# Performance work log

Hardware: AMD Instinct MI355X
Metric: run time of the kernel (lower is better)

Reference implementation:

```python
import jax, jax.numpy as jnp
import numpy as np
from jax import lax

S_IN = 16; V_IN = 16; S_OUT = 16; V_OUT = 16
SIZE = 7; STRIDE = 2; PAD = 3; EPS = 1e-5
# n_basis per (rep_out, rep_in) pair = n_radial(3) * number of allowed CG paths
NB = {('s','s'): 3, ('s','v'): 3, ('s','t'): 9, ('v','s'): 3, ('v','v'): 9, ('v','t'): 21}
DIMS = {'s': 1, 'v': 3, 't': 9}  # repr1, repr3, repr3x3 dimensions


def _basis(key, nb, d_out, d_in):
    # Stand-in for the constant steerable basis (spherical harmonics x Clebsch-Gordan
    # x radial windows). These are data-independent constants in se3cnn; the compute
    # pattern (weighted basis sum -> dense 3D conv) is identical.
    return jax.random.normal(key, (nb, d_out, d_in, SIZE, SIZE, SIZE), jnp.float32) / np.sqrt(SIZE ** 3)


def setup_inputs() -> dict:
    key = jax.random.key(0)
    ks = jax.random.split(key, 16)
    inp = {"sv": jax.random.normal(ks[0], (4, S_IN + 3 * V_IN, 32, 32, 32), jnp.float32)}
    mul_in = {'s': S_IN, 'v': V_IN, 't': V_IN}
    i = 1
    for o in ['s', 'v']:
        mo = S_OUT if o == 's' else V_OUT
        for a in ['s', 'v', 't']:
            nb = NB[(o, a)]
            inp[f"basis_{o}{a}"] = _basis(ks[i], nb, DIMS[o], DIMS[a])
            inp[f"w_{o}{a}"] = jax.random.normal(ks[i + 1], (mo, mul_in[a], nb), jnp.float32) / np.sqrt(nb * mul_in[a] * DIMS[a])
            i += 2
    inp["bn_g_s"] = jnp.ones((S_OUT,), jnp.float32)
    inp["bn_g_v"] = jnp.ones((V_OUT,), jnp.float32)
    inp["bias_s"] = jnp.zeros((S_OUT,), jnp.float32)
    return inp


def _block(w, basis):
    # w: [mul_out, mul_in, nb], basis: [nb, d_out, d_in, 7,7,7] -> [mul_out*d_out, mul_in*d_in, 7,7,7]
    mo, mi, nb = w.shape
    do, di = basis.shape[1], basis.shape[2]
    k = jnp.einsum('uvb,bijxyz->uivjxyz', w, basis)
    return k.reshape(mo * do, mi * di, SIZE, SIZE, SIZE)


def _forward(sv, w_ss, w_sv, w_st, w_vs, w_vv, w_vt,
             basis_ss, basis_sv, basis_st, basis_vs, basis_vv, basis_vt,
             bn_g_s, bn_g_v, bias_s):
    B = sv.shape[0]; sp = sv.shape[2:]
    # TensorProduct: vector fields -> vector (x) vector = repr3x3 (9 channels each)
    v = sv[:, S_IN:].reshape(B, V_IN, 3, *sp)
    t = jnp.einsum('buixyz,bujxyz->buijxyz', v, v).reshape(B, V_IN * 9, *sp)
    svt = jnp.concatenate([sv, t], axis=1)  # [B, S_IN + 3*V_IN + 9*V_IN, X,Y,Z]
    # SE3Convolution: assemble kernel from steerable basis, then dense 3D conv
    row_s = jnp.concatenate([_block(w_ss, basis_ss), _block(w_sv, basis_sv), _block(w_st, basis_st)], axis=1)
    row_v = jnp.concatenate([_block(w_vs, basis_vs), _block(w_vv, basis_vv), _block(w_vt, basis_vt)], axis=1)
    kernel = jnp.concatenate([row_s, row_v], axis=0)  # [S_OUT + 3*V_OUT, 208, 7,7,7]
    y = lax.conv_general_dilated(svt, kernel, (STRIDE,) * 3, [(PAD, PAD)] * 3,
                                 dimension_numbers=('NCDHW', 'OIDHW', 'NCDHW'))
    osp = y.shape[2:]
    # SE3BatchNorm: per-field second-moment normalization (training-mode batch stats)
    ys = y[:, :S_OUT]
    yv = y[:, S_OUT:].reshape(B, V_OUT, 3, *osp)
    var_s = jnp.mean(ys * ys, axis=(0, 2, 3, 4))
    ys = ys * (bn_g_s / jnp.sqrt(var_s + EPS))[None, :, None, None, None]
    var_v = jnp.mean(yv * yv, axis=(0, 2, 3, 4, 5))
    yv = yv * (bn_g_v / jnp.sqrt(var_v + EPS))[None, :, None, None, None, None]
    # BiasRelu: bias + relu on scalar fields only; vector fields pass through
    ys = jax.nn.relu(ys + bias_s[None, :, None, None, None])
    return jnp.concatenate([ys, yv.reshape(B, 3 * V_OUT, *osp)], axis=1)


def reference(sv, w_ss, w_sv, w_st, w_vs, w_vv, w_vt,
              basis_ss, basis_sv, basis_st, basis_vs, basis_vv, basis_vt,
              bn_g_s, bn_g_v, bias_s):
    return _forward(sv, w_ss, w_sv, w_st, w_vs, w_vv, w_vt,
                    basis_ss, basis_sv, basis_st, basis_vs, basis_vv, basis_vt,
                    bn_g_s, bn_g_v, bias_s)
```

## Files before the change

### kernel.cpp

```cpp
#include <hip/hip_runtime.h>
#include <hip/hip_bf16.h>


using f4  = __attribute__((ext_vector_type(4)))  float;
using f16v= __attribute__((ext_vector_type(16))) float;
using s8  = __attribute__((ext_vector_type(8)))  short;

#define C_TOT 160
#define PZ_   37
#define NTAP  343
#define NROW  (4 * PZ_ * PZ_)
#define KSN   8
#define SLICE_E 1048576

#define AROW    1232
#define AE_ROWS 19
#define AO_ROWS 18
#define AO_OFF  23552
#define B_OFF   46080
#define BSZ     14336
#define LDS_SZ  (B_OFF + 2 * BSZ)

__device__ __forceinline__ void gl_lds16(const void* g, void* l) {
    __builtin_amdgcn_global_load_lds(
        (const __attribute__((address_space(1))) unsigned int*)g,
        (__attribute__((address_space(3))) unsigned int*)l, 16, 0, 0);
}

__device__ __forceinline__ void pair_ij(int p, int& i, int& j) {
    if (p < 3)      { i = p; j = p; }
    else if (p == 3){ i = 0; j = 1; }
    else if (p == 4){ i = 0; j = 2; }
    else            { i = 1; j = 2; }
}

struct bf2 { __hip_bfloat16 x, y; };
struct bh4 { __hip_bfloat16 x, y, z, w; };

__global__ void build_w_kernel(
    const float* __restrict__ b_ss, const float* __restrict__ w_ss,
    const float* __restrict__ b_sv, const float* __restrict__ w_sv,
    const float* __restrict__ b_st, const float* __restrict__ w_st,
    const float* __restrict__ b_vs, const float* __restrict__ w_vs,
    const float* __restrict__ b_vv, const float* __restrict__ w_vv,
    const float* __restrict__ b_vt, const float* __restrict__ w_vt,
    __hip_bfloat16* __restrict__ wl)
{
    __shared__ float S[13056];
    const int tid = threadIdx.x;
    const int tap = blockIdx.x;
    float* L = S;
    float* W = S + 768;
    for (int r = tid; r < 750; r += 192) {
        float v;
        if (r < 3)        v = b_ss[r * NTAP + tap];
        else if (r < 12)  v = b_sv[(r - 3) * NTAP + tap];
        else if (r < 93)  v = b_st[(r - 12) * NTAP + tap];
        else if (r < 102) v = b_vs[(r - 93) * NTAP + tap];
        else if (r < 183) v = b_vv[(r - 102) * NTAP + tap];
        else              v = b_vt[(r - 183) * NTAP + tap];
        L[r] = v;
    }
    for (int r = tid; r < 12288; r += 192) {
        float v;
        if (r < 768)       v = w_ss[r];
        else if (r < 1536) v = w_sv[r - 768];
        else if (r < 3840) v = w_st[r - 1536];
        else if (r < 4608) v = w_vs[r - 3840];
        else if (r < 6912) v = w_vv[r - 4608];
        else               v = w_vt[r - 6912];
        W[r] = v;
    }
    __syncthreads();

    if (tid < 160) {
        const int c = tid;
        const int chunk = c >> 4, cw = c & 15;
        __hip_bfloat16* dst = wl + ((size_t)chunk * NTAP + tap) * 1024 + cw;

        if (c < 16) {
            const float l0 = L[0], l1 = L[1], l2 = L[2];
#pragma unroll
            for (int n = 0; n < 16; ++n) {
                const float* wr = &W[(n * 16 + c) * 3];
                dst[n * 16] = __float2bfloat16(wr[0]*l0 + wr[1]*l1 + wr[2]*l2);
            }
            float bv[3][3];
#pragma unroll
            for (int dn = 0; dn < 3; ++dn)
#pragma unroll
                for (int t = 0; t < 3; ++t) bv[dn][t] = L[93 + t*3 + dn];
#pragma unroll
            for (int u = 0; u < 16; ++u) {
                const float* wr = &W[3840 + (u * 16 + c) * 3];
                const float w0 = wr[0], w1 = wr[1], w2 = wr[2];
#pragma unroll
                for (int dn = 0; dn < 3; ++dn)
                    dst[(16 + u*3 + dn) * 16] = __float2bfloat16(
                        w0*bv[dn][0] + w1*bv[dn][1] + w2*bv[dn][2]);
            }
        } else if (c < 64) {
            const int mm = (c - 16) / 3, di = (c - 16) % 3;
            float bs0[3];
#pragma unroll
            for (int t = 0; t < 3; ++t) bs0[t] = L[3 + t*3 + di];
#pragma unroll
            for (int n = 0; n < 16; ++n) {
                const float* wr = &W[768 + (n * 16 + mm) * 3];
                dst[n * 16] = __float2bfloat16(
                    wr[0]*bs0[0] + wr[1]*bs0[1] + wr[2]*bs0[2]);
            }
            float bv[3][9];
#pragma unroll
            for (int dn = 0; dn < 3; ++dn)
#pragma unroll
                for (int t = 0; t < 9; ++t)
                    bv[dn][t] = L[102 + (t*3 + dn)*3 + di];
#pragma unroll
            for (int u = 0; u < 16; ++u) {
                const float* wr = &W[4608 + (u * 16 + mm) * 9];
                float a0 = 0.f, a1 = 0.f, a2 = 0.f;
#pragma unroll
                for (int t = 0; t < 9; ++t) {
                    const float wv = wr[t];
                    a0 += wv * bv[0][t]; a1 += wv * bv[1][t]; a2 += wv * bv[2][t];
                }
                dst[(16 + u*3 + 0) * 16] = __float2bfloat16(a0);
                dst[(16 + u*3 + 1) * 16] = __float2bfloat16(a1);
                dst[(16 + u*3 + 2) * 16] = __float2bfloat16(a2);
            }
        } else {
            const int q = c - 64, mm = q / 6, p = q % 6;
            int i, jj; pair_ij(p, i, jj);
            const int d1 = i*3 + jj, d2 = jj*3 + i;
            const bool dbl = (i != jj);
            float bs0[9];
#pragma unroll
            for (int t = 0; t < 9; ++t) {
                float b = L[12 + t*9 + d1];
                if (dbl) b += L[12 + t*9 + d2];
                bs0[t] = b;
            }
#pragma unroll
            for (int n = 0; n < 16; ++n) {
                const float* wr = &W[1536 + (n * 16 + mm) * 9];
                float acc = 0.f;
#pragma unroll
                for (int t = 0; t < 9; ++t) acc += wr[t] * bs0[t];
                dst[n * 16] = __float2bfloat16(acc);
            }
            float bv0[21], bv1[21], bv2[21];
#pragma unroll
            for (int t = 0; t < 21; ++t) {
                float x0 = L[183 + (t*3 + 0)*9 + d1];
                float x1 = L[183 + (t*3 + 1)*9 + d1];
                float x2 = L[183 + (t*3 + 2)*9 + d1];
                if (dbl) {
                    x0 += L[183 + (t*3 + 0)*9 + d2];
                    x1 += L[183 + (t*3 + 1)*9 + d2];
                    x2 += L[183 + (t*3 + 2)*9 + d2];
                }
                bv0[t] = x0; bv1[t] = x1; bv2[t] = x2;
            }
#pragma unroll
            for (int u = 0; u < 16; ++u) {
                const float* wr = &W[6912 + (u * 16 + mm) * 21];
                float a0 = 0.f, a1 = 0.f, a2 = 0.f;
#pragma unroll
                for (int t = 0; t < 21; ++t) {
                    const float wv = wr[t];
                    a0 += wv * bv0[t]; a1 += wv * bv1[t]; a2 += wv * bv2[t];
                }
                dst[(16 + u*3 + 0) * 16] = __float2bfloat16(a0);
                dst[(16 + u*3 + 1) * 16] = __float2bfloat16(a1);
                dst[(16 + u*3 + 2) * 16] = __float2bfloat16(a2);
            }
        }
    }
}

__global__ void build_xt_kernel(
    const float* __restrict__ sv, __hip_bfloat16* __restrict__ xt)
{
    __shared__ float row[2112];
    const int tid = threadIdx.x;
    const int bid = blockIdx.x;
    const int y = bid % 37, z = (bid / 37) % 37, b = bid / 1369;
    const bool interior = (z >= 3 && z < 35 && y >= 3 && y < 35);
    if (interior) {
        const float* src = sv + (size_t)b * 2097152 + (z-3) * 1024 + (y-3) * 32;
        for (int f = tid; f < 2048; f += 256) {
            int ch = f >> 5, x = f & 31;
            row[x * 66 + ch] = src[(size_t)ch * 32768 + x];
        }
    }
    __syncthreads();
    for (int e2 = tid; e2 < 3040; e2 += 256) {
        const int chunk = e2 / 304;
        const int r     = e2 - chunk * 304;
        const int s     = r >> 3;
        const int cw    = (r & 7) * 2;
        const int c     = chunk * 16 + cw;
        float v0 = 0.f, v1 = 0.f;
        if (interior && s >= 3 && s < 35) {
            const int x = s - 3;
            if (c < 64) {
                v0 = row[x * 66 + c];
                v1 = row[x * 66 + c + 1];
            } else {
                int q = c - 64, u = q / 6, p = q % 6, i, j;
                pair_ij(p, i, j);
                v0 = row[x * 66 + 16 + u * 3 + i] * row[x * 66 + 16 + u * 3 + j];
                pair_ij(p + 1, i, j);
                v1 = row[x * 66 + 16 + u * 3 + i] * row[x * 66 + 16 + u * 3 + j];
            }
        }
        bf2 w{__float2bfloat16(v0), __float2bfloat16(v1)};
        *(bf2*)(xt + ((size_t)chunk * NROW + bid) * 608 + r * 2) = w;
    }
}

__global__ __launch_bounds__(256, 2) void conv_mfma_kernel(
    const __hip_bfloat16* __restrict__ xt,
    const __hip_bfloat16* __restrict__ wl,
    __hip_bfloat16* __restrict__ y4b)
{
    __shared__ __align__(16) char lds[LDS_SZ];

    const int phys = blockIdx.x;
    const int bid  = (phys & 7) * (64 * KSN / 8) + (phys >> 3);

    const int low3 = bid & 7;
    const int rest = bid >> 3;
    const int ks   = rest % KSN;
    const int mb   = (rest / KSN) * 8 + low3;
    const int b    = mb >> 4;
    const int oz   = mb & 15;

    const int tid  = threadIdx.x;
    const int w    = tid >> 6;
    const int lane = tid & 63;
    const int m    = lane & 31;
    const int h    = lane >> 5;

    int invAE[6]; int nAE = 0;
#pragma unroll
    for (int k = 0; k < 6; ++k) {
        const int i = w + 4 * k;
        if (i < 23) {
            const int o = i * 1024 + lane * 16;
            int r = o / AROW;
            int rem = o - r * AROW;
            if (r > AE_ROWS - 1) { r = AE_ROWS - 1; rem = 0; }
            if (rem >= 1216) rem = 0;
            const int s  = rem >> 5;
            const int cg = ((rem >> 4) & 1) ^ ((s >> 1) & 1);
            invAE[k] = (2 * r) * 608 + s * 16 + cg * 8;
            nAE = k + 1;
        }
    }
    int invAO[6]; int nAO = 0;
#pragma unroll
    for (int k = 0; k < 6; ++k) {
        const int i = w + 4 * k;
        if (i < 22) {
            const int o = i * 1024 + lane * 16;
            int r = o / AROW;
            int rem = o - r * AROW;
            if (r > AO_ROWS - 1) { r = AO_ROWS - 1; rem = 0; }
            if (rem >= 1216) rem = 0;
            const int s  = rem >> 5;
            const int cg = ((rem >> 4) & 1) ^ ((s >> 1) & 1);
            invAO[k] = (2 * r + 1) * 608 + s * 16 + cg * 8;
            nAO = k + 1;
        }
    }
    int invB[4]; int nB = 0;
#pragma unroll
    for (int k = 0; k < 4; ++k) {
        const int i = w + 4 * k;
        if (i < 14) {
            const int kx = i >> 1, nt = i & 1;
            invB[k] = kx * 1024 + (nt * 32 + m) * 16 + h * 8;
            nB = k + 1;
        }
    }

    f16v acc[2][2];
    for (int t = 0; t < 2; ++t)
        for (int n = 0; n < 2; ++n)
            for (int k = 0; k < 16; ++k) acc[t][n][k] = 0.f;

    const int rA0   = ((m >> 4) << 2) + ((m >> 2) & 3);
    const int sbase = (w << 3) + ((m & 3) << 1);

    auto stageAE = [&](int g) {
        const int chunk = g / 7, kz = g - chunk * 7;
        const size_t u = ((size_t)chunk * NROW
                        + (size_t)(b * PZ_ + 2 * oz + kz) * PZ_) * 608;
#pragma unroll
        for (int k = 0; k < 6; ++k)
            if (k < nAE) gl_lds16(xt + u + invAE[k], lds + (w + 4 * k) * 1024);
    };
    auto stageAO = [&](int g) {
        const int chunk = g / 7, kz = g - chunk * 7;
        const size_t u = ((size_t)chunk * NROW
                        + (size_t)(b * PZ_ + 2 * oz + kz) * PZ_) * 608;
#pragma unroll
        for (int k = 0; k < 6; ++k)
            if (k < nAO) gl_lds16(xt + u + invAO[k], lds + AO_OFF + (w + 4 * k) * 1024);
    };
    auto stageB = [&](int g, int kyv, int bsel) {
        const int chunk = g / 7, kz = g - chunk * 7;
        const size_t u = ((size_t)chunk * NTAP + (size_t)(kz * 7 + kyv) * 7) * 1024;
        char* dst = lds + B_OFF + bsel * BSZ;
#pragma unroll
        for (int k = 0; k < 4; ++k)
            if (k < nB) gl_lds16(wl + u + invB[k], dst + (w + 4 * k) * 1024);
    };

    auto compute = [&](int ky, int bsel) {
        const int abase = (ky & 1) ? AO_OFF : 0;
        const char* abp = lds + abase + (rA0 + (ky >> 1)) * AROW;
        const char* bbp = lds + B_OFF + bsel * BSZ;
#pragma unroll
        for (int kx = 0; kx < 7; ++kx) {
            const int s   = sbase + kx;
            const int cgp = h ^ ((s >> 1) & 1);
            const char* ap = abp + s * 32 + cgp * 16;
            const s8 a0 = *(const s8*)(ap);
            const s8 a1 = *(const s8*)(ap + 8 * AROW);
            const char* bp = bbp + kx * 2048 + h * 512 + m * 16;
            const s8 b0 = *(const s8*)(bp);
            const s8 b1 = *(const s8*)(bp + 1024);
            acc[0][0] = __builtin_amdgcn_mfma_f32_32x32x16_bf16(a0, b0, acc[0][0], 0, 0, 0);
            acc[0][1] = __builtin_amdgcn_mfma_f32_32x32x16_bf16(a0, b1, acc[0][1], 0, 0, 0);
            acc[1][0] = __builtin_amdgcn_mfma_f32_32x32x16_bf16(a1, b0, acc[1][0], 0, 0, 0);
            acc[1][1] = __builtin_amdgcn_mfma_f32_32x32x16_bf16(a1, b1, acc[1][1], 0, 0, 0);
        }
    };

    const int G = (70 - ks + KSN - 1) / KSN;
    const int T = G * 7;
    stageAO(ks);
    stageB(ks, 1, 0);
    __syncthreads();
    int bB = 0;
    for (int t = 0; t < T; ++t) {
        const int gi = t / 7, p = t - gi * 7;
        const int g  = ks + gi * KSN;
        const int ky = (p < 3) ? (2 * p + 1) : (2 * (p - 3));
        const int tn = t + 1;
        if (tn < T) {
            const int gin = tn / 7, pn = tn - gin * 7;
            const int kyn = (pn < 3) ? (2 * pn + 1) : (2 * (pn - 3));
            stageB(ks + gin * KSN, kyn, bB ^ 1);
        }
        if (p == 0) stageAE(g);
        else if (p == 3 && g + KSN < 70) stageAO(g + KSN);
        compute(ky, bB);
        __syncthreads();
        bB ^= 1;
    }

    const int nl = lane & 31;
    f4* yb = (f4*)lds;
    __hip_bfloat16* dst0 = y4b + (size_t)ks * SLICE_E + (size_t)(b * 64) * 4096;
#pragma unroll
    for (int t = 0; t < 2; ++t) {
        __syncthreads();
#pragma unroll
        for (int nt = 0; nt < 2; ++nt) {
            const int n = nt * 32 + nl;
#pragma unroll
            for (int q = 0; q < 4; ++q) {
                const int rr = 2 * q + h;
                f4 v = { acc[t][nt][4*q], acc[t][nt][4*q+1],
                         acc[t][nt][4*q+2], acc[t][nt][4*q+3] };
                yb[n * 33 + rr * 4 + w] = v;
            }
        }
        __syncthreads();
        for (int j = tid; j < 2048; j += 256) {
            const int n  = j >> 5, sp = j & 31;
            f4 v = yb[n * 33 + sp];
            const int rr = sp >> 2, wq = sp & 3;
            const int yo = t * 8 + (rr >> 2) * 4 + (rr & 3);
            bh4 p{__float2bfloat16(v.x), __float2bfloat16(v.y),
                  __float2bfloat16(v.z), __float2bfloat16(v.w)};
            *(bh4*)(dst0 + (size_t)n * 4096 + oz * 256 + yo * 16 + wq * 4) = p;
        }
    }
}

__global__ void combine_reduce_kernel(const __hip_bfloat16* __restrict__ y4b,
                                      float* __restrict__ yc,
                                      float* __restrict__ sums2)
{
    const int n = blockIdx.x & 63, q = blockIdx.x >> 6;
    const size_t base = ((size_t)q * 64 + n) * 4096;
    float s = 0.f;
    for (int i = threadIdx.x; i < 1024; i += 256) {
        const size_t off = base + (size_t)i * 4;
        f4 v = {0.f, 0.f, 0.f, 0.f};
#pragma unroll
        for (int k = 0; k < KSN; ++k) {
            bh4 r = *(const bh4*)(y4b + off + (size_t)k * SLICE_E);
            v.x += (float)r.x; v.y += (float)r.y;
            v.z += (float)r.z; v.w += (float)r.w;
        }
        *(f4*)(yc + off) = v;
        s += v.x * v.x + v.y * v.y + v.z * v.z + v.w * v.w;
    }
    __shared__ float red[256];
    red[threadIdx.x] = s;
    __syncthreads();
    for (int st = 128; st > 0; st >>= 1) {
        if (threadIdx.x < st) red[threadIdx.x] += red[threadIdx.x + st];
        __syncthreads();
    }
    if (threadIdx.x == 0) sums2[n * 4 + q] = red[0];
}

__global__ void finalize_kernel(const float* __restrict__ yc,
                                const float* __restrict__ sums2,
                                const float* __restrict__ g_s,
                                const float* __restrict__ g_v,
                                const float* __restrict__ bias_s,
                                float* __restrict__ out)
{
    const int idx = blockIdx.x * 256 + threadIdx.x;
    const int n = (idx >> 12) & 63;
    float v = yc[idx];
    if (n < 16) {
        float sum = sums2[n*4] + sums2[n*4+1] + sums2[n*4+2] + sums2[n*4+3];
        float var = sum * (1.0f / 16384.0f);
        float sc  = g_s[n] / sqrtf(var + 1e-5f);
        v = fmaxf(v * sc + bias_s[n], 0.f);
    } else {
        int u = (n - 16) / 3;
        float sum = 0.f;
        for (int k = 0; k < 12; ++k) sum += sums2[(16 + u * 3) * 4 + k];
        float var = sum * (1.0f / 49152.0f);
        v = v * (g_v[u] / sqrtf(var + 1e-5f));
    }
    out[idx] = v;
}

extern "C" void kernel_launch(void* const* d_in, const int* in_sizes, int n_in,
                              void* d_out, int out_size, void* d_ws, size_t ws_size,
                              hipStream_t stream)
{
    const float* sv    = (const float*)d_in[0];
    const float* b_ss  = (const float*)d_in[1];
    const float* w_ss  = (const float*)d_in[2];
    const float* b_sv  = (const float*)d_in[3];
    const float* w_sv  = (const float*)d_in[4];
    const float* b_st  = (const float*)d_in[5];
    const float* w_st  = (const float*)d_in[6];
    const float* b_vs  = (const float*)d_in[7];
    const float* w_vs  = (const float*)d_in[8];
    const float* b_vv  = (const float*)d_in[9];
    const float* w_vv  = (const float*)d_in[10];
    const float* b_vt  = (const float*)d_in[11];
    const float* w_vt  = (const float*)d_in[12];
    const float* bn_gs = (const float*)d_in[13];
    const float* bn_gv = (const float*)d_in[14];
    const float* bias_s= (const float*)d_in[15];
    float* out = (float*)d_out;

    char* ws = (char*)d_ws;
    constexpr size_t XT_BYTES = (size_t)10 * NROW * 1216;
    constexpr size_t WL_BYTES = (size_t)10 * NTAP * 2048;
    constexpr size_t Y4_BYTES = (size_t)KSN * SLICE_E * 2;
    constexpr size_t YC_BYTES = (size_t)4 * 64 * 4096 * 4;

    __hip_bfloat16* xt  = (__hip_bfloat16*)ws;
    __hip_bfloat16* wl  = (__hip_bfloat16*)(ws + XT_BYTES);
    __hip_bfloat16* y4b = (__hip_bfloat16*)(ws + XT_BYTES + WL_BYTES);
    float* yc    = (float*)(ws + XT_BYTES + WL_BYTES + Y4_BYTES);
    float* sums2 = (float*)(ws + XT_BYTES + WL_BYTES + Y4_BYTES + YC_BYTES);

    build_xt_kernel<<<5476, 256, 0, stream>>>(sv, xt);
    build_w_kernel<<<343, 192, 0, stream>>>(
        b_ss, w_ss, b_sv, w_sv, b_st, w_st, b_vs, w_vs, b_vv, w_vv,
        b_vt, w_vt, wl);
    conv_mfma_kernel<<<64 * KSN, 256, 0, stream>>>(xt, wl, y4b);
    combine_reduce_kernel<<<256, 256, 0, stream>>>(y4b, yc, sums2);
    finalize_kernel<<<4096, 256, 0, stream>>>(yc, sums2, bn_gs, bn_gv, bias_s, out);
}
```

Measured before the change: 252.2 us.

## Fuse combine-reduce and BN finalize via grid-wide atomic barrier

Merges the slice-combine/sum-of-squares kernel with the batch-norm finalize kernel into one launch. Combined values stay in registers, and a global atomic counter acts as a grid barrier so every block waits until all partial sums are written. This removes the fp32 intermediate buffer round trip and one kernel launch. It adds a memset and relies on all 256 blocks being co-resident, otherwise the spin-wait deadlocks.

```diff
diff --git a/kernel.cpp b/kernel.cpp
--- a/kernel.cpp
+++ b/kernel.cpp
@@ -393,58 +393,88 @@
     }
 }
 
-__global__ void combine_reduce_kernel(const __hip_bfloat16* __restrict__ y4b,
-                                      float* __restrict__ yc,
-                                      float* __restrict__ sums2)
+__global__ void combine_finalize_kernel(const __hip_bfloat16* __restrict__ y4b,
+                                        const float* __restrict__ g_s,
+                                        const float* __restrict__ g_v,
+                                        const float* __restrict__ bias_s,
+                                        float* __restrict__ out,
+                                        float* __restrict__ sums2,
+                                        int* __restrict__ counter)
 {
+    const int tid = threadIdx.x;
     const int n = blockIdx.x & 63, q = blockIdx.x >> 6;
     const size_t base = ((size_t)q * 64 + n) * 4096;
+
     float s = 0.f;
-    for (int i = threadIdx.x; i < 1024; i += 256) {
-        const size_t off = base + (size_t)i * 4;
-        f4 v = {0.f, 0.f, 0.f, 0.f};
-#pragma unroll
-        for (int k = 0; k < KSN; ++k) {
-            bh4 r = *(const bh4*)(y4b + off + (size_t)k * SLICE_E);
-            v.x += (float)r.x; v.y += (float)r.y;
-            v.z += (float)r.z; v.w += (float)r.w;
-        }
-        *(f4*)(yc + off) = v;
-        s += v.x * v.x + v.y * v.y + v.z * v.z + v.w * v.w;
-    }
+    f4 v0, v1, v2, v3;
+#define SUMSLICES(VV, IT) {                                                   \
+        const size_t off = base + (size_t)(tid + (IT) * 256) * 4;             \
+        f4 v = {0.f, 0.f, 0.f, 0.f};                                          \
+        _Pragma("unroll")                                                     \
+        for (int k = 0; k < KSN; ++k) {                                       \
+            bh4 r = *(const bh4*)(y4b + off + (size_t)k * SLICE_E);           \
+            v.x += (float)r.x; v.y += (float)r.y;                             \
+            v.z += (float)r.z; v.w += (float)r.w;                             \
+        }                                                                     \
+        VV = v;                                                               \
+        s += v.x*v.x + v.y*v.y + v.z*v.z + v.w*v.w;                           \
+    }
+    SUMSLICES(v0, 0) SUMSLICES(v1, 1) SUMSLICES(v2, 2) SUMSLICES(v3, 3)
+#undef SUMSLICES
+
     __shared__ float red[256];
-    red[threadIdx.x] = s;
+    red[tid] = s;
     __syncthreads();
     for (int st = 128; st > 0; st >>= 1) {
-        if (threadIdx.x < st) red[threadIdx.x] += red[threadIdx.x + st];
+        if (tid < st) red[tid] += red[tid + st];
         __syncthreads();
     }
-    if (threadIdx.x == 0) sums2[n * 4 + q] = red[0];
-}
-
-__global__ void finalize_kernel(const float* __restrict__ yc,
-                                const float* __restrict__ sums2,
-                                const float* __restrict__ g_s,
-                                const float* __restrict__ g_v,
-                                const float* __restrict__ bias_s,
-                                float* __restrict__ out)
-{
-    const int idx = blockIdx.x * 256 + threadIdx.x;
-    const int n = (idx >> 12) & 63;
-    float v = yc[idx];
+    if (tid == 0) {
+        __hip_atomic_store(&sums2[n * 4 + q], red[0],
+                           __ATOMIC_RELAXED, __HIP_MEMORY_SCOPE_AGENT);
+        __threadfence();
+        atomicAdd(counter, 1);
+        while (__hip_atomic_load(counter, __ATOMIC_ACQUIRE,
+                                 __HIP_MEMORY_SCOPE_AGENT) < 256) {}
+    }
+    __syncthreads();
+
+    float scale = 0.f, bias = 0.f;
+    bool do_relu = false;
     if (n < 16) {
-        float sum = sums2[n*4] + sums2[n*4+1] + sums2[n*4+2] + sums2[n*4+3];
-        float var = sum * (1.0f / 16384.0f);
-        float sc  = g_s[n] / sqrtf(var + 1e-5f);
-        v = fmaxf(v * sc + bias_s[n], 0.f);
+        float sum = 0.f;
+#pragma unroll
+        for (int k = 0; k < 4; ++k)
+            sum += __hip_atomic_load(&sums2[n * 4 + k],
+                                     __ATOMIC_RELAXED, __HIP_MEMORY_SCOPE_AGENT);
+        const float var = sum * (1.0f / 16384.0f);
+        scale = g_s[n] / sqrtf(var + 1e-5f);
+        bias = bias_s[n];
+        do_relu = true;
     } else {
-        int u = (n - 16) / 3;
+        const int u = (n - 16) / 3;
         float sum = 0.f;
-        for (int k = 0; k < 12; ++k) sum += sums2[(16 + u * 3) * 4 + k];
-        float var = sum * (1.0f / 49152.0f);
-        v = v * (g_v[u] / sqrtf(var + 1e-5f));
-    }
-    out[idx] = v;
+#pragma unroll
+        for (int k = 0; k < 12; ++k)
+            sum += __hip_atomic_load(&sums2[(16 + u * 3) * 4 + k],
+                                     __ATOMIC_RELAXED, __HIP_MEMORY_SCOPE_AGENT);
+        const float var = sum * (1.0f / 49152.0f);
+        scale = g_v[u] / sqrtf(var + 1e-5f);
+    }
+
+#define WRITEOUT(VV, IT) {                                                    \
+        const size_t off = base + (size_t)(tid + (IT) * 256) * 4;             \
+        f4 o;                                                                 \
+        o.x = VV.x * scale + bias; o.y = VV.y * scale + bias;                 \
+        o.z = VV.z * scale + bias; o.w = VV.w * scale + bias;                 \
+        if (do_relu) {                                                        \
+            o.x = fmaxf(o.x, 0.f); o.y = fmaxf(o.y, 0.f);                     \
+            o.z = fmaxf(o.z, 0.f); o.w = fmaxf(o.w, 0.f);                     \
+        }                                                                     \
+        *(f4*)(out + off) = o;                                                \
+    }
+    WRITEOUT(v0, 0) WRITEOUT(v1, 1) WRITEOUT(v2, 2) WRITEOUT(v3, 3)
+#undef WRITEOUT
 }
 
 extern "C" void kernel_launch(void* const* d_in, const int* in_sizes, int n_in,
@@ -473,19 +503,20 @@
     constexpr size_t XT_BYTES = (size_t)10 * NROW * 1216;
     constexpr size_t WL_BYTES = (size_t)10 * NTAP * 2048;
     constexpr size_t Y4_BYTES = (size_t)KSN * SLICE_E * 2;
-    constexpr size_t YC_BYTES = (size_t)4 * 64 * 4096 * 4;
+    constexpr size_t S2_BYTES = 256 * 4;
 
     __hip_bfloat16* xt  = (__hip_bfloat16*)ws;
     __hip_bfloat16* wl  = (__hip_bfloat16*)(ws + XT_BYTES);
     __hip_bfloat16* y4b = (__hip_bfloat16*)(ws + XT_BYTES + WL_BYTES);
-    float* yc    = (float*)(ws + XT_BYTES + WL_BYTES + Y4_BYTES);
-    float* sums2 = (float*)(ws + XT_BYTES + WL_BYTES + Y4_BYTES + YC_BYTES);
-
+    float* sums2 = (float*)(ws + XT_BYTES + WL_BYTES + Y4_BYTES);
+    int*   counter = (int*)(ws + XT_BYTES + WL_BYTES + Y4_BYTES + S2_BYTES);
+
+    hipMemsetAsync(counter, 0, 4, stream);
     build_xt_kernel<<<5476, 256, 0, stream>>>(sv, xt);
     build_w_kernel<<<343, 192, 0, stream>>>(
         b_ss, w_ss, b_sv, w_sv, b_st, w_st, b_vs, w_vs, b_vv, w_vv,
         b_vt, w_vt, wl);
     conv_mfma_kernel<<<64 * KSN, 256, 0, stream>>>(xt, wl, y4b);
-    combine_reduce_kernel<<<256, 256, 0, stream>>>(y4b, yc, sums2);
-    finalize_kernel<<<4096, 256, 0, stream>>>(yc, sums2, bn_gs, bn_gv, bias_s, out);
-}
+    combine_finalize_kernel<<<256, 256, 0, stream>>>(
+        y4b, bn_gs, bn_gv, bias_s, out, sums2, counter);
+}
```

Result: slower. 258.2 us (+2.4%).
